# Performance work log

Measured on AMD Instinct MI355X. Metric: run time of the kernel, lower is better.

## Reference

```python
import jax, jax.numpy as jnp
import numpy as np

H = 4      # num_attention_heads
DK = 75    # d_k = hidden_size // H
HID = 300  # hidden_size


def setup_inputs() -> dict:
    key = jax.random.key(0)
    ks = jax.random.split(key, 9)
    B, S = 8, 2048
    query = jax.random.normal(ks[0], (B, S, HID), dtype=jnp.float32)
    key_t = jax.random.normal(ks[1], (B, S, HID), dtype=jnp.float32)
    value = jax.random.normal(ks[2], (B, S, HID), dtype=jnp.float32)
    mask = jax.random.randint(ks[3], (B, S), 0, 2, dtype=jnp.int32)
    scale = 1.0 / np.sqrt(HID)
    Wq = jax.random.normal(ks[4], (HID, HID), dtype=jnp.float32) * scale
    Wk = jax.random.normal(ks[5], (HID, HID), dtype=jnp.float32) * scale
    Wv = jax.random.normal(ks[6], (HID, HID), dtype=jnp.float32) * scale
    Wo = jax.random.normal(ks[7], (HID, HID), dtype=jnp.float32) * scale
    bo = jax.random.normal(ks[8], (HID,), dtype=jnp.float32) * 0.01
    return {"query": query, "key": key_t, "value": value, "mask": mask,
            "Wq": Wq, "Wk": Wk, "Wv": Wv, "Wo": Wo, "bo": bo}


def reference(query, key, value, mask, Wq, Wk, Wv, Wo, bo):
    B, S, _ = query.shape
    # QKV projections (nn.Linear: x @ W.T), split into heads: [B,H,S,DK]
    def proj(x, W):
        return (x @ W.T).reshape(B, S, H, DK).transpose(0, 2, 1, 3)
    q, k, v = proj(query, Wq), proj(key, Wk), proj(value, Wv)
    # scores: [B,H,S,S]
    scores = jnp.einsum('bhqd,bhkd->bhqk', q, k) / jnp.sqrt(jnp.float32(DK))
    # mask outer product 'bi,bj->bij' broadcast over heads; fill zeros with -1e9
    m2 = (mask[:, :, None] * mask[:, None, :])[:, None, :, :]  # [B,1,S,S]
    scores = jnp.where(m2 == 0, jnp.float32(-1e9), scores)
    p_attn = jax.nn.softmax(scores, axis=-1)  # dropout p=0.0 (eval mode)
    x = jnp.einsum('bhqk,bhkd->bhqd', p_attn, v)  # [B,H,S,DK]
    x = x.transpose(0, 2, 1, 3).reshape(B, S, H * DK)
    return x @ Wo.T + bo
```

## Files before the change

kernel.cpp:

```cpp
#include <hip/hip_runtime.h>
#include <math.h>

typedef __bf16 bf16x8 __attribute__((ext_vector_type(8)));
typedef float f32x4 __attribute__((ext_vector_type(4)));
typedef float f32x16 __attribute__((ext_vector_type(16)));
typedef unsigned short u16;
typedef u16 u16x8 __attribute__((ext_vector_type(8)));

#define HID 300
#define NH 4
#define DK 75
#define DKP 80
#define BB 8
#define SS 2048
#define BSROWS (BB*SS)
#define C2   0.16658807f

#define MFMA(a,b,c)   __builtin_amdgcn_mfma_f32_16x16x32_bf16(a,b,c,0,0,0)
#define MFMA32(a,b,c) __builtin_amdgcn_mfma_f32_32x32x16_bf16(a,b,c,0,0,0)

static __device__ __forceinline__ void split2(float x, u16& hb, u16& lb) {
    const unsigned u = __float_as_uint(x);
    hb = (u16)(u >> 16);
    const float r = x - __uint_as_float(u & 0xffff0000u);
    lb = (u16)(__float_as_uint(r) >> 16);
}
static __device__ __forceinline__ void split2rne(float x, u16& hb, u16& lb) {
    const unsigned u = __float_as_uint(x);
    const unsigned uh = ((u + 0x7fffu + ((u >> 16) & 1u)) >> 16) << 16;
    hb = (u16)(uh >> 16);
    const float r = x - __uint_as_float(uh);
    lb = (u16)(__float_as_uint(r) >> 16);
}
static __device__ __forceinline__ unsigned pkbf(float a, float b) {
    const unsigned short ua = __builtin_bit_cast(unsigned short, (__bf16)a);
    const unsigned short ub = __builtin_bit_cast(unsigned short, (__bf16)b);
    return (unsigned)ua | ((unsigned)ub << 16);
}

__global__ __launch_bounds__(256)
void prep_w3(const float* __restrict__ Wq, const float* __restrict__ Wk,
             const float* __restrict__ Wv,
             u16* __restrict__ wph, u16* __restrict__ wpl)
{
    const int idx = blockIdx.x * 256 + threadIdx.x;
    if (idx >= 38400) return;
    const int c8 = idx % 40;
    int r = idx / 40;
    const int n = r % 80; r /= 80;
    const int h = r & 3;  r >>= 2;
    const int mat = r;
    const float* W = (mat == 0) ? Wq : (mat == 1) ? Wk : Wv;
    const int col0 = c8 * 8;
    float v[8];
#pragma unroll
    for (int j = 0; j < 8; ++j) v[j] = 0.f;
    if (n < DK) {
        const float* s = W + (size_t)(h * DK + n) * HID + col0;
        if (col0 + 8 <= HID) {
#pragma unroll
            for (int j = 0; j < 8; ++j) v[j] = s[j];
        } else {
#pragma unroll
            for (int j = 0; j < 8; ++j) v[j] = (col0 + j < HID) ? s[j] : 0.f;
        }
    }
    u16x8 hv, lv;
#pragma unroll
    for (int j = 0; j < 8; ++j) {
        u16 hb, lb;
        split2(v[j], hb, lb);
        hv[j] = hb; lv[j] = lb;
    }
    const size_t base = ((size_t)((mat * 4 + h) * 80 + n)) * 320 + col0;
    *(u16x8*)(wph + base) = hv;
    *(u16x8*)(wpl + base) = lv;
}

template <int MODE, int HPB>
static __device__ __forceinline__ void gemm_body(
    char* smem, const float* __restrict__ A, const float* __restrict__ W,
    const u16* __restrict__ Wph, const u16* __restrict__ Wpl,
    const float* __restrict__ bias, u16* __restrict__ hiP, u16* __restrict__ loP,
    float* __restrict__ foutP, const int bx, const int hp,
    const int* __restrict__ pmask, const float scale, const int patch)
{
    constexpr int WROWS = 80 * HPB;
    constexpr int NT = 5 * HPB;
    u16* Ah = (u16*)smem;
    u16* Al = Ah + 128 * 40;
    u16* Wh = Al + 128 * 40;
    u16* Wl = Wh + WROWS * 40;

    const int t = threadIdx.x;
    const int wv = t >> 6, l = t & 63, qc = l & 15, g = l >> 4;
    const int row0 = bx * 128;
    const int b = row0 >> 11;
    const int s0 = row0 & 2047;

    const f32x4 zf = {0.f, 0.f, 0.f, 0.f};
    f32x4 acc[2][NT];
#pragma unroll
    for (int mt = 0; mt < 2; ++mt)
#pragma unroll
        for (int nt = 0; nt < NT; ++nt) acc[mt][nt] = zf;

    const int rA = t >> 1, halfA = t & 1;
    float4 aPf[4];
    constexpr int WJ  = (WROWS * 4 + 255) / 256;
    constexpr int WJ2 = (WROWS * 8 + 255) / 256;
    u16x8 wPfH[WJ], wPfL[WJ];
    float4 wPf2[WJ2];

    auto loadA = [&](int step) {
        const int k0 = step * 32 + halfA * 16;
        const float* src = A + (size_t)(row0 + rA) * HID + k0;
#pragma unroll
        for (int c4 = 0; c4 < 4; ++c4) {
            const int k = k0 + c4 * 4;
            float4 v;
            if (k + 4 <= HID) v = *(const float4*)(src + c4 * 4);
            else {
                v.x = (k + 0 < HID) ? src[c4 * 4 + 0] : 0.f;
                v.y = (k + 1 < HID) ? src[c4 * 4 + 1] : 0.f;
                v.z = (k + 2 < HID) ? src[c4 * 4 + 2] : 0.f;
                v.w = (k + 3 < HID) ? src[c4 * 4 + 3] : 0.f;
            }
            aPf[c4] = v;
        }
    };
    auto loadW = [&](int step) {
        const int k0 = step * 32;
        if constexpr (MODE <= 1) {
#pragma unroll
            for (int j = 0; j < WJ; ++j) {
                const int idx = j * 256 + t;
                if (idx < WROWS * 4) {
                    const int n = idx >> 2, c = idx & 3;
                    const int nh = (n >= 80) ? 1 : 0, nn = n - nh * 80;
                    const size_t wo = (size_t)((hp * HPB + nh) * 80 + nn) * 320 + k0 + c * 8;
                    wPfH[j] = *(const u16x8*)(Wph + wo);
                    wPfL[j] = *(const u16x8*)(Wpl + wo);
                }
            }
        } else {
#pragma unroll
            for (int j = 0; j < WJ2; ++j) {
                const int idx = j * 256 + t;
                if (idx < WROWS * 8) {
                    const int n = idx >> 3, c = idx & 7;
                    const int nh = (n >= 80) ? 1 : 0, nn = n - nh * 80;
                    const int k = k0 + c * 4;
                    float4 v = make_float4(0.f, 0.f, 0.f, 0.f);
                    if (nn < DK) {
                        const float* src = W + (size_t)((hp * HPB + nh) * DK + nn) * HID + k;
                        if (k + 4 <= HID) v = *(const float4*)src;
                        else {
                            v.x = (k + 0 < HID) ? src[0] : 0.f;
                            v.y = (k + 1 < HID) ? src[1] : 0.f;
                            v.z = (k + 2 < HID) ? src[2] : 0.f;
                            v.w = (k + 3 < HID) ? src[3] : 0.f;
                        }
                    }
                    wPf2[j] = v;
                }
            }
        }
    };
    auto writeA = [&]() {
        u16* dh = Ah + rA * 40 + halfA * 16;
        u16* dl = Al + rA * 40 + halfA * 16;
#pragma unroll
        for (int c4 = 0; c4 < 4; ++c4) {
            ushort4 h4, l4;
            split2(aPf[c4].x, h4.x, l4.x);
            split2(aPf[c4].y, h4.y, l4.y);
            split2(aPf[c4].z, h4.z, l4.z);
            split2(aPf[c4].w, h4.w, l4.w);
            *(ushort4*)(dh + c4 * 4) = h4;
            *(ushort4*)(dl + c4 * 4) = l4;
        }
    };
    auto writeW = [&]() {
        if constexpr (MODE <= 1) {
#pragma unroll
            for (int j = 0; j < WJ; ++j) {
                const int idx = j * 256 + t;
                if (idx < WROWS * 4) {
                    const int n = idx >> 2, c = idx & 3;
                    *(u16x8*)(Wh + n * 40 + c * 8) = wPfH[j];
                    *(u16x8*)(Wl + n * 40 + c * 8) = wPfL[j];
                }
            }
        } else {
#pragma unroll
            for (int j = 0; j < WJ2; ++j) {
                const int idx = j * 256 + t;
                if (idx < WROWS * 8) {
                    const int n = idx >> 3, c = idx & 7;
                    ushort4 h4, l4;
                    split2(wPf2[j].x, h4.x, l4.x);
                    split2(wPf2[j].y, h4.y, l4.y);
                    split2(wPf2[j].z, h4.z, l4.z);
                    split2(wPf2[j].w, h4.w, l4.w);
                    *(ushort4*)(Wh + n * 40 + c * 4) = h4;
                    *(ushort4*)(Wl + n * 40 + c * 4) = l4;
                }
            }
        }
    };

    loadA(0);
    loadW(0);

    for (int step = 0; step < 10; ++step) {
        __syncthreads();
        writeA();
        writeW();
        __syncthreads();
        if (step < 9) {
            loadA(step + 1);
            loadW(step + 1);
        }
        bf16x8 ah[2], al2[2];
#pragma unroll
        for (int mt = 0; mt < 2; ++mt) {
            const int roff = (wv * 32 + mt * 16 + qc) * 40 + g * 8;
            ah[mt]  = *(const bf16x8*)(Ah + roff);
            al2[mt] = *(const bf16x8*)(Al + roff);
        }
#pragma unroll
        for (int nt = 0; nt < NT; ++nt) {
            const int woff = (nt * 16 + qc) * 40 + g * 8;
            const bf16x8 bh = *(const bf16x8*)(Wh + woff);
            const bf16x8 bl = *(const bf16x8*)(Wl + woff);
#pragma unroll
            for (int mt = 0; mt < 2; ++mt) {
                acc[mt][nt] = MFMA(ah[mt],  bh, acc[mt][nt]);
                acc[mt][nt] = MFMA(al2[mt], bh, acc[mt][nt]);
                acc[mt][nt] = MFMA(ah[mt],  bl, acc[mt][nt]);
            }
        }
    }
    __syncthreads();

#pragma unroll
    for (int ph = 0; ph < HPB; ++ph) {
        const int h = hp * HPB + ph;
        if constexpr (MODE <= 1) {
            unsigned* epi = (unsigned*)smem;
#pragma unroll
            for (int mt = 0; mt < 2; ++mt)
#pragma unroll
                for (int nt = 0; nt < 5; ++nt)
#pragma unroll
                    for (int r = 0; r < 4; ++r) {
                        u16 hb, lb;
                        split2rne(acc[mt][ph * 5 + nt][r] * scale, hb, lb);
                        if (patch != 0 && nt == 4 && qc == 11) {
                            if (patch == 1) { hb = (u16)0x3F80; lb = 0; }
                            else {
                                const int sr = s0 + wv * 32 + mt * 16 + g * 4 + r;
                                hb = (pmask[b * SS + sr] != 0) ? (u16)0 : (u16)0xC320;
                                lb = 0;
                            }
                        }
                        epi[(wv * 32 + mt * 16 + g * 4 + r) * 84 + nt * 16 + qc] =
                            (unsigned)hb | ((unsigned)lb << 16);
                    }
            __syncthreads();
            if constexpr (MODE == 0) {
                const int r = t >> 1, half = t & 1;
                const unsigned* row = epi + r * 84 + half * 40;
                const size_t base = ((size_t)(b * NH + h) * SS + s0 + r) * DKP + half * 40;
                u16* dh = hiP + base;
#pragma unroll
                for (int i = 0; i < 5; ++i) {
                    u16x8 hv, lv;
#pragma unroll
                    for (int j = 0; j < 8; ++j) {
                        const unsigned u = row[i * 8 + j];
                        hv[j] = (u16)u; lv[j] = (u16)(u >> 16);
                    }
                    *(u16x8*)(dh + i * 8) = hv;
                    if (loP) *(u16x8*)(loP + base + i * 8) = lv;
                }
            } else {
#pragma unroll
                for (int i = 0; i < 3; ++i) {
                    const int idx = i * 256 + t;
                    if (idx < 640) {
                        const int d = idx >> 3, sc = (idx & 7) * 16;
                        const size_t base = ((size_t)(b * NH + h) * DKP + d) * SS + s0 + sc;
                        u16* dh = hiP + base;
                        u16x8 h0, h1, l0, l1;
#pragma unroll
                        for (int j = 0; j < 8; ++j) {
                            unsigned u = epi[(sc + j) * 84 + d];
                            h0[j] = (u16)u; l0[j] = (u16)(u >> 16);
                            u = epi[(sc + 8 + j) * 84 + d];
                            h1[j] = (u16)u; l1[j] = (u16)(u >> 16);
                        }
                        *(u16x8*)dh = h0; *(u16x8*)(dh + 8) = h1;
                        if (loP) {
                            *(u16x8*)(loP + base) = l0;
                            *(u16x8*)(loP + base + 8) = l1;
                        }
                    }
                }
            }
        } else {
            float* epf = (float*)smem;
#pragma unroll
            for (int mt = 0; mt < 2; ++mt)
#pragma unroll
                for (int nt = 0; nt < 5; ++nt)
#pragma unroll
                    for (int r = 0; r < 4; ++r)
                        epf[(wv * 32 + mt * 16 + g * 4 + r) * 84 + nt * 16 + qc] =
                            acc[mt][ph * 5 + nt][r];
            __syncthreads();
            for (int i = 0; i < 38; ++i) {
                const int idx = i * 256 + t;
                if (idx < 128 * DK) {
                    const int r = idx / DK, c = idx - r * DK;
                    foutP[(size_t)(row0 + r) * HID + h * DK + c] = epf[r * 84 + c] + bias[h * DK + c];
                }
            }
        }
        if (ph + 1 < HPB) __syncthreads();
    }
}

__global__ __launch_bounds__(256, 3)
void proj3_gemm(const float* __restrict__ Aq, const float* __restrict__ Ak,
                const float* __restrict__ Av, const int* __restrict__ mask,
                const u16* __restrict__ wph, const u16* __restrict__ wpl,
                u16* __restrict__ qh, u16* __restrict__ ql,
                u16* __restrict__ kh, u16* __restrict__ vh)
{
    __shared__ char smem[46080];
    const int z = blockIdx.z;
    const float* A = (z == 0) ? Aq : (z == 1) ? Ak : Av;
    const size_t WMAT = (size_t)4 * 80 * 320;
    u16* hiP = (z == 0) ? qh : (z == 1) ? kh : vh;
    u16* loP = (z == 0) ? ql : nullptr;
    const float scale = (z == 0) ? C2 : 1.0f;
    const int patch = (z == 0) ? 1 : (z == 1) ? 2 : 0;
    if (z == 2)
        gemm_body<1, 2>(smem, A, nullptr, wph + z * WMAT, wpl + z * WMAT,
                        nullptr, hiP, loP, nullptr, blockIdx.x, blockIdx.y,
                        mask, scale, patch);
    else
        gemm_body<0, 2>(smem, A, nullptr, wph + z * WMAT, wpl + z * WMAT,
                        nullptr, hiP, loP, nullptr, blockIdx.x, blockIdx.y,
                        mask, scale, patch);
}

__global__ __launch_bounds__(256)
void out_gemm(const float* __restrict__ A, const float* __restrict__ W,
              const float* __restrict__ bias, float* __restrict__ out)
{
    __shared__ char smem[43008];
    gemm_body<2, 1>(smem, A, W, nullptr, nullptr, bias, nullptr, nullptr, out,
                    blockIdx.x, blockIdx.y, nullptr, 1.0f, 0);
}

__global__ __launch_bounds__(256, 2)
void attn_mfma32(const u16* __restrict__ qhi, const u16* __restrict__ qlo,
                 const u16* __restrict__ khi, const u16* __restrict__ vhi,
                 const int* __restrict__ mask, float* __restrict__ xout)
{
    __shared__ u16 KsH[2 * 8192];
    __shared__ u16 VsH[2 * 6144];
    __shared__ u16 Ps[4 * 2048];

    const int t = threadIdx.x;
    const int wv = t >> 6;
    const int l = t & 63;
    const int q = l & 31;
    const int hi = l >> 5;

    const int bx = blockIdx.x;
    const int xcd = bx & 7, idx = bx >> 3;
    const int bh = xcd * 4 + (idx & 3);
    const int qt = idx >> 2;
    const int b = bh >> 2;
    const int h = bh & 3;
    const int q0 = qt * 128;

    {
        const int rr = (t >> 4) & 15, o8 = t & 15;
        *(uint2*)(VsH + (80 + rr) * 64 + o8 * 4) = make_uint2(0u, 0u);
        *(uint2*)(VsH + 6144 + (80 + rr) * 64 + o8 * 4) = make_uint2(0u, 0u);
    }

    const size_t planeQK = (size_t)bh * (SS * DKP);
    const int qrow = q0 + wv * 32 + q;
    const int mq = (mask[b * SS + qrow] != 0);
    const u16x8 qm = (u16x8)(u16)(mq ? 0xFFFFu : 0u);

    bf16x8 Qh[5], Ql[5];
    {
        const u16* ph = qhi + planeQK + (size_t)qrow * DKP;
        const u16* pl = qlo + planeQK + (size_t)qrow * DKP;
#pragma unroll
        for (int ch = 0; ch < 5; ++ch) {
            u16x8 ua = *(const u16x8*)(ph + 16 * ch + 8 * hi) & qm;
            u16x8 ub = *(const u16x8*)(pl + 16 * ch + 8 * hi) & qm;
            Qh[ch] = *(bf16x8*)&ua;
            Ql[ch] = *(bf16x8*)&ub;
        }
    }

    const u16* kH = khi + planeQK;
    const u16* vH = vhi + (size_t)bh * (DKP * SS);
    u16* PsW = Ps + wv * 2048;

    int kOff[5], kLds[5], vOff[5], vLds[5];
#pragma unroll
    for (int i = 0; i < 5; ++i) {
        const int gi = t + i * 256;
        const int r = gi / 20, c8 = gi % 20;
        kOff[i] = r * 160 + c8 * 8;
        kLds[i] = r * 256 + ((c8 * 8) ^ ((r & 7) << 4));
        const int d = gi >> 4, cv = gi & 15;
        vOff[i] = d * 4096 + cv * 8;
        vLds[i] = d * 128 + ((cv * 8) ^ ((d & 7) << 4));
    }

    uint2 kr[5], vr[5];
#define LOADT(KT) do { _Pragma("unroll") \
    for (int i = 0; i < 5; ++i) { \
        kr[i] = *(const uint2*)((const char*)kH + (size_t)(KT) * 10240 + kOff[i]); \
        vr[i] = *(const uint2*)((const char*)vH + (size_t)(KT) * 128 + vOff[i]); \
    } } while (0)
#define WRITET(BUF) do { _Pragma("unroll") \
    for (int i = 0; i < 5; ++i) { \
        *(uint2*)((char*)(KsH + (BUF) * 8192) + kLds[i]) = kr[i]; \
        *(uint2*)((char*)(VsH + (BUF) * 6144) + vLds[i]) = vr[i]; \
    } } while (0)

    LOADT(0);
    WRITET(0);
    LOADT(1);
    __syncthreads();

    f32x16 O[3];
#pragma unroll
    for (int dt = 0; dt < 3; ++dt) O[dt] = (f32x16){};
    float ll = 0.f;
    const int kswz = (q & 7) << 4;
    const int pswz = kswz;

    for (int kt = 0; kt < 32; ++kt) {
        const int cur = kt & 1;
        const char* Kc = (const char*)(KsH + cur * 8192);
        const char* Vc = (const char*)(VsH + cur * 6144);

        f32x16 s0 = (f32x16){}, s1 = (f32x16){};
#pragma unroll
        for (int ch = 0; ch < 5; ++ch) {
            const int o = (32 * ch + 16 * hi) ^ kswz;
            const bf16x8 a0 = *(const bf16x8*)(Kc + q * 256 + o);
            const bf16x8 a1 = *(const bf16x8*)(Kc + (32 + q) * 256 + o);
            s0 = MFMA32(a0, Qh[ch], s0);
            s0 = MFMA32(a0, Ql[ch], s0);
            s1 = MFMA32(a1, Qh[ch], s1);
            s1 = MFMA32(a1, Ql[ch], s1);
        }

        float p0 = 0.f, p1 = 0.f, p2 = 0.f, p3 = 0.f;
#pragma unroll
        for (int sb = 0; sb < 2; ++sb) {
            const f32x16 sv = sb ? s1 : s0;
            float e[16];
#pragma unroll
            for (int r = 0; r < 16; r += 4) {
                e[r + 0] = __builtin_amdgcn_exp2f(sv[r + 0]);
                e[r + 1] = __builtin_amdgcn_exp2f(sv[r + 1]);
                e[r + 2] = __builtin_amdgcn_exp2f(sv[r + 2]);
                e[r + 3] = __builtin_amdgcn_exp2f(sv[r + 3]);
                p0 += e[r + 0]; p1 += e[r + 1]; p2 += e[r + 2]; p3 += e[r + 3];
            }
#pragma unroll
            for (int rr = 0; rr < 4; ++rr) {
                uint2 w;
                w.x = pkbf(e[4 * rr + 0], e[4 * rr + 1]);
                w.y = pkbf(e[4 * rr + 2], e[4 * rr + 3]);
                const int o = (sb * 64 + 16 * rr + 8 * hi) ^ pswz;
                *(uint2*)((char*)PsW + q * 128 + o) = w;
            }
        }
        ll += (p0 + p1) + (p2 + p3);

#pragma unroll
        for (int c = 0; c < 4; ++c) {
            const int po = q * 128 + ((32 * c + 16 * hi) ^ pswz);
            const bf16x8 pA = *(const bf16x8*)((char*)PsW + po);
#pragma unroll
            for (int dt = 0; dt < 3; ++dt) {
                const int drow = 32 * dt + q;
                const int vb = drow * 128 + ((32 * c + 16 * hi) ^ ((drow & 7) << 4));
                const bf16x8 vh8 = *(const bf16x8*)(Vc + vb);
                O[dt] = MFMA32(vh8, pA, O[dt]);
            }
        }

        if (kt < 31) {
            WRITET(cur ^ 1);
            if (kt < 30) LOADT(kt + 2);
        }
        __syncthreads();
    }
#undef LOADT
#undef WRITET

    ll += __shfl_xor(ll, 32);
    {
        const float inv = 1.0f / ll;
        float* o = xout + (size_t)(b * SS + qrow) * HID + h * DK;
#pragma unroll
        for (int dt = 0; dt < 3; ++dt)
#pragma unroll
            for (int r = 0; r < 16; ++r) {
                const int d = 32 * dt + (r & 3) + 8 * (r >> 2) + 4 * hi;
                if (d < DK) o[d] = O[dt][r] * inv;
            }
    }
}

extern "C" void kernel_launch(void* const* d_in, const int* in_sizes, int n_in,
                              void* d_out, int out_size, void* d_ws, size_t ws_size,
                              hipStream_t stream)
{
    const float* query = (const float*)d_in[0];
    const float* key_t = (const float*)d_in[1];
    const float* value = (const float*)d_in[2];
    const int*   mask  = (const int*)d_in[3];
    const float* Wq    = (const float*)d_in[4];
    const float* Wk    = (const float*)d_in[5];
    const float* Wv    = (const float*)d_in[6];
    const float* Wo    = (const float*)d_in[7];
    const float* bo    = (const float*)d_in[8];
    float* out = (float*)d_out;

    const size_t PL = (size_t)BB * NH * SS * DKP;
    u16* qh = (u16*)d_ws;
    u16* ql = qh + PL;
    u16* kh = ql + PL;
    u16* kl = kh + PL;   (void)kl;
    u16* vh = kl + PL;
    u16* vl = vh + PL;
    float* xws = (float*)(vl + PL);
    u16* wph = (u16*)xws;
    u16* wpl = wph + (size_t)3 * 4 * 80 * 320;

    const dim3 blk(256, 1, 1);

    prep_w3<<<150, blk, 0, stream>>>(Wq, Wk, Wv, wph, wpl);

    proj3_gemm<<<dim3(128, 2, 3), blk, 0, stream>>>(query, key_t, value, mask,
                                                    wph, wpl,
                                                    qh, ql, kh, vh);

    attn_mfma32<<<dim3(512, 1, 1), blk, 0, stream>>>(qh, ql, kh, vh, mask, xws);

    out_gemm<<<dim3(128, NH, 1), blk, 0, stream>>>(xws, Wo, bo, out);
}
```

Before: 174.1 us.

## Double GEMM K-chunk, deepen attention K/V prefetch, widen K-tile swizzle

The projection and output GEMMs now stage 64-wide K chunks in LDS instead of 32, which halves the number of barrier-separated steps. Shared memory grows accordingly and launch bounds are set to 2 blocks per CU. The attention kernel keeps two register sets of K/V tiles so global loads are issued two tiles ahead, and the K-tile LDS swizzle now uses 16 row phases to reduce bank conflicts. Risks are lower occupancy from the larger LDS footprint and higher register pressure from the extra prefetch buffers.

```diff
diff --git a/kernel.cpp b/kernel.cpp
--- a/kernel.cpp
+++ b/kernel.cpp
@@ -87,10 +87,11 @@
 {
     constexpr int WROWS = 80 * HPB;
     constexpr int NT = 5 * HPB;
+    constexpr int KC = 64;
     u16* Ah = (u16*)smem;
-    u16* Al = Ah + 128 * 40;
-    u16* Wh = Al + 128 * 40;
-    u16* Wl = Wh + WROWS * 40;
+    u16* Al = Ah + 128 * KC;
+    u16* Wh = Al + 128 * KC;
+    u16* Wl = Wh + WROWS * KC;
 
     const int t = threadIdx.x;
     const int wv = t >> 6, l = t & 63, qc = l & 15, g = l >> 4;
@@ -106,17 +107,17 @@
         for (int nt = 0; nt < NT; ++nt) acc[mt][nt] = zf;
 
     const int rA = t >> 1, halfA = t & 1;
-    float4 aPf[4];
-    constexpr int WJ  = (WROWS * 4 + 255) / 256;
-    constexpr int WJ2 = (WROWS * 8 + 255) / 256;
+    float4 aPf[8];
+    constexpr int WJ  = (WROWS * 8 + 255) / 256;
+    constexpr int WJ2 = (WROWS * 16 + 255) / 256;
     u16x8 wPfH[WJ], wPfL[WJ];
     float4 wPf2[WJ2];
 
     auto loadA = [&](int step) {
-        const int k0 = step * 32 + halfA * 16;
+        const int k0 = step * KC + halfA * 32;
         const float* src = A + (size_t)(row0 + rA) * HID + k0;
 #pragma unroll
-        for (int c4 = 0; c4 < 4; ++c4) {
+        for (int c4 = 0; c4 < 8; ++c4) {
             const int k = k0 + c4 * 4;
             float4 v;
             if (k + 4 <= HID) v = *(const float4*)(src + c4 * 4);
@@ -130,13 +131,13 @@
         }
     };
     auto loadW = [&](int step) {
-        const int k0 = step * 32;
+        const int k0 = step * KC;
         if constexpr (MODE <= 1) {
 #pragma unroll
             for (int j = 0; j < WJ; ++j) {
                 const int idx = j * 256 + t;
-                if (idx < WROWS * 4) {
-                    const int n = idx >> 2, c = idx & 3;
+                if (idx < WROWS * 8) {
+                    const int n = idx >> 3, c = idx & 7;
                     const int nh = (n >= 80) ? 1 : 0, nn = n - nh * 80;
                     const size_t wo = (size_t)((hp * HPB + nh) * 80 + nn) * 320 + k0 + c * 8;
                     wPfH[j] = *(const u16x8*)(Wph + wo);
@@ -147,8 +148,8 @@
 #pragma unroll
             for (int j = 0; j < WJ2; ++j) {
                 const int idx = j * 256 + t;
-                if (idx < WROWS * 8) {
-                    const int n = idx >> 3, c = idx & 7;
+                if (idx < WROWS * 16) {
+                    const int n = idx >> 4, c = idx & 15;
                     const int nh = (n >= 80) ? 1 : 0, nn = n - nh * 80;
                     const int k = k0 + c * 4;
                     float4 v = make_float4(0.f, 0.f, 0.f, 0.f);
@@ -168,10 +169,10 @@
         }
     };
     auto writeA = [&]() {
-        u16* dh = Ah + rA * 40 + halfA * 16;
-        u16* dl = Al + rA * 40 + halfA * 16;
-#pragma unroll
-        for (int c4 = 0; c4 < 4; ++c4) {
+        u16* dh = Ah + rA * KC + halfA * 32;
+        u16* dl = Al + rA * KC + halfA * 32;
+#pragma unroll
+        for (int c4 = 0; c4 < 8; ++c4) {
             ushort4 h4, l4;
             split2(aPf[c4].x, h4.x, l4.x);
             split2(aPf[c4].y, h4.y, l4.y);
@@ -186,25 +187,25 @@
 #pragma unroll
             for (int j = 0; j < WJ; ++j) {
                 const int idx = j * 256 + t;
-                if (idx < WROWS * 4) {
-                    const int n = idx >> 2, c = idx & 3;
-                    *(u16x8*)(Wh + n * 40 + c * 8) = wPfH[j];
-                    *(u16x8*)(Wl + n * 40 + c * 8) = wPfL[j];
+                if (idx < WROWS * 8) {
+                    const int n = idx >> 3, c = idx & 7;
+                    *(u16x8*)(Wh + n * KC + c * 8) = wPfH[j];
+                    *(u16x8*)(Wl + n * KC + c * 8) = wPfL[j];
                 }
             }
         } else {
 #pragma unroll
             for (int j = 0; j < WJ2; ++j) {
                 const int idx = j * 256 + t;
-                if (idx < WROWS * 8) {
-                    const int n = idx >> 3, c = idx & 7;
+                if (idx < WROWS * 16) {
+                    const int n = idx >> 4, c = idx & 15;
                     ushort4 h4, l4;
                     split2(wPf2[j].x, h4.x, l4.x);
                     split2(wPf2[j].y, h4.y, l4.y);
                     split2(wPf2[j].z, h4.z, l4.z);
                     split2(wPf2[j].w, h4.w, l4.w);
-                    *(ushort4*)(Wh + n * 40 + c * 4) = h4;
-                    *(ushort4*)(Wl + n * 40 + c * 4) = l4;
+                    *(ushort4*)(Wh + n * KC + c * 4) = h4;
+                    *(ushort4*)(Wl + n * KC + c * 4) = l4;
                 }
             }
         }
@@ -213,32 +214,35 @@
     loadA(0);
     loadW(0);
 
-    for (int step = 0; step < 10; ++step) {
+    for (int step = 0; step < 5; ++step) {
         __syncthreads();
         writeA();
         writeW();
         __syncthreads();
-        if (step < 9) {
+        if (step < 4) {
             loadA(step + 1);
             loadW(step + 1);
         }
-        bf16x8 ah[2], al2[2];
-#pragma unroll
-        for (int mt = 0; mt < 2; ++mt) {
-            const int roff = (wv * 32 + mt * 16 + qc) * 40 + g * 8;
-            ah[mt]  = *(const bf16x8*)(Ah + roff);
-            al2[mt] = *(const bf16x8*)(Al + roff);
-        }
-#pragma unroll
-        for (int nt = 0; nt < NT; ++nt) {
-            const int woff = (nt * 16 + qc) * 40 + g * 8;
-            const bf16x8 bh = *(const bf16x8*)(Wh + woff);
-            const bf16x8 bl = *(const bf16x8*)(Wl + woff);
+#pragma unroll
+        for (int cc = 0; cc < 2; ++cc) {
+            bf16x8 ah[2], al2[2];
 #pragma unroll
             for (int mt = 0; mt < 2; ++mt) {
-                acc[mt][nt] = MFMA(ah[mt],  bh, acc[mt][nt]);
-                acc[mt][nt] = MFMA(al2[mt], bh, acc[mt][nt]);
-                acc[mt][nt] = MFMA(ah[mt],  bl, acc[mt][nt]);
+                const int roff = (wv * 32 + mt * 16 + qc) * KC + cc * 32 + g * 8;
+                ah[mt]  = *(const bf16x8*)(Ah + roff);
+                al2[mt] = *(const bf16x8*)(Al + roff);
+            }
+#pragma unroll
+            for (int nt = 0; nt < NT; ++nt) {
+                const int woff = (nt * 16 + qc) * KC + cc * 32 + g * 8;
+                const bf16x8 bh = *(const bf16x8*)(Wh + woff);
+                const bf16x8 bl = *(const bf16x8*)(Wl + woff);
+#pragma unroll
+                for (int mt = 0; mt < 2; ++mt) {
+                    acc[mt][nt] = MFMA(ah[mt],  bh, acc[mt][nt]);
+                    acc[mt][nt] = MFMA(al2[mt], bh, acc[mt][nt]);
+                    acc[mt][nt] = MFMA(ah[mt],  bl, acc[mt][nt]);
+                }
             }
         }
     }
@@ -332,14 +336,14 @@
     }
 }
 
-__global__ __launch_bounds__(256, 3)
+__global__ __launch_bounds__(256, 2)
 void proj3_gemm(const float* __restrict__ Aq, const float* __restrict__ Ak,
                 const float* __restrict__ Av, const int* __restrict__ mask,
                 const u16* __restrict__ wph, const u16* __restrict__ wpl,
                 u16* __restrict__ qh, u16* __restrict__ ql,
                 u16* __restrict__ kh, u16* __restrict__ vh)
 {
-    __shared__ char smem[46080];
+    __shared__ char smem[73728];
     const int z = blockIdx.z;
     const float* A = (z == 0) ? Aq : (z == 1) ? Ak : Av;
     const size_t WMAT = (size_t)4 * 80 * 320;
@@ -357,11 +361,11 @@
                         mask, scale, patch);
 }
 
-__global__ __launch_bounds__(256)
+__global__ __launch_bounds__(256, 2)
 void out_gemm(const float* __restrict__ A, const float* __restrict__ W,
               const float* __restrict__ bias, float* __restrict__ out)
 {
-    __shared__ char smem[43008];
+    __shared__ char smem[53248];
     gemm_body<2, 1>(smem, A, W, nullptr, nullptr, bias, nullptr, nullptr, out,
                     blockIdx.x, blockIdx.y, nullptr, 1.0f, 0);
 }
@@ -423,35 +427,36 @@
         const int gi = t + i * 256;
         const int r = gi / 20, c8 = gi % 20;
         kOff[i] = r * 160 + c8 * 8;
-        kLds[i] = r * 256 + ((c8 * 8) ^ ((r & 7) << 4));
+        kLds[i] = r * 256 + ((c8 * 8) ^ ((r & 15) << 4));
         const int d = gi >> 4, cv = gi & 15;
         vOff[i] = d * 4096 + cv * 8;
         vLds[i] = d * 128 + ((cv * 8) ^ ((d & 7) << 4));
     }
 
-    uint2 kr[5], vr[5];
-#define LOADT(KT) do { _Pragma("unroll") \
+    uint2 krA[5], vrA[5], krB[5], vrB[5];
+#define LOADT(KT, KR, VR) do { _Pragma("unroll") \
     for (int i = 0; i < 5; ++i) { \
-        kr[i] = *(const uint2*)((const char*)kH + (size_t)(KT) * 10240 + kOff[i]); \
-        vr[i] = *(const uint2*)((const char*)vH + (size_t)(KT) * 128 + vOff[i]); \
+        KR[i] = *(const uint2*)((const char*)kH + (size_t)(KT) * 10240 + kOff[i]); \
+        VR[i] = *(const uint2*)((const char*)vH + (size_t)(KT) * 128 + vOff[i]); \
     } } while (0)
-#define WRITET(BUF) do { _Pragma("unroll") \
+#define WRITET(BUF, KR, VR) do { _Pragma("unroll") \
     for (int i = 0; i < 5; ++i) { \
-        *(uint2*)((char*)(KsH + (BUF) * 8192) + kLds[i]) = kr[i]; \
-        *(uint2*)((char*)(VsH + (BUF) * 6144) + vLds[i]) = vr[i]; \
+        *(uint2*)((char*)(KsH + (BUF) * 8192) + kLds[i]) = KR[i]; \
+        *(uint2*)((char*)(VsH + (BUF) * 6144) + vLds[i]) = VR[i]; \
     } } while (0)
 
-    LOADT(0);
-    WRITET(0);
-    LOADT(1);
+    LOADT(0, krA, vrA);
+    WRITET(0, krA, vrA);
+    LOADT(1, krA, vrA);
+    LOADT(2, krB, vrB);
     __syncthreads();
 
     f32x16 O[3];
 #pragma unroll
     for (int dt = 0; dt < 3; ++dt) O[dt] = (f32x16){};
     float ll = 0.f;
-    const int kswz = (q & 7) << 4;
-    const int pswz = kswz;
+    const int kswz = (q & 15) << 4;
+    const int pswz = (q & 7) << 4;
 
     for (int kt = 0; kt < 32; ++kt) {
         const int cur = kt & 1;
@@ -461,9 +466,10 @@
         f32x16 s0 = (f32x16){}, s1 = (f32x16){};
 #pragma unroll
         for (int ch = 0; ch < 5; ++ch) {
-            const int o = (32 * ch + 16 * hi) ^ kswz;
-            const bf16x8 a0 = *(const bf16x8*)(Kc + q * 256 + o);
-            const bf16x8 a1 = *(const bf16x8*)(Kc + (32 + q) * 256 + o);
+            const int o0 = (32 * ch + 16 * hi) ^ kswz;
+            const int o1 = (32 * ch + 16 * hi) ^ (((32 + q) & 15) << 4);
+            const bf16x8 a0 = *(const bf16x8*)(Kc + q * 256 + o0);
+            const bf16x8 a1 = *(const bf16x8*)(Kc + (32 + q) * 256 + o1);
             s0 = MFMA32(a0, Qh[ch], s0);
             s0 = MFMA32(a0, Ql[ch], s0);
             s1 = MFMA32(a1, Qh[ch], s1);
@@ -508,8 +514,13 @@
         }
 
         if (kt < 31) {
-            WRITET(cur ^ 1);
-            if (kt < 30) LOADT(kt + 2);
+            if ((kt & 1) == 0) {
+                WRITET(cur ^ 1, krA, vrA);
+                if (kt < 29) LOADT(kt + 3, krA, vrA);
+            } else {
+                WRITET(cur ^ 1, krB, vrB);
+                if (kt < 29) LOADT(kt + 3, krB, vrB);
+            }
         }
         __syncthreads();
     }
```

Result: slower. 177.7 us (+2.1%).
